# Optimization experiments

Measured on AMD Instinct MI355X. Metric: run time of the kernel, lower is better.

The kernel has to match this reference:

```python
import jax, jax.numpy as jnp
import numpy as np

ALIGN_CORNERS = True
APPLY_SMOOTHSTEP = True

SIZES = [(32, 32, 32), (64, 64, 64), (128, 128, 128), (256, 256, 256)]
FEAT_DIMS = [4, 4, 4, 4]
N_POINTS = 1048576  # 2**20 sample points (e.g. 8192 rays x 128 samples)


def setup_inputs() -> dict:
    key = jax.random.key(0)
    ks = jax.random.split(key, 1 + len(SIZES))
    # grid_sample-style coords in [-1, 1], layout [1, 1, 1, N, 3] (x, y, z)
    grid = jax.random.uniform(ks[0], (1, 1, 1, N_POINTS, 3), dtype=jnp.float32) * 2.0 - 1.0
    inp = {"grid": grid}
    for i, (size, c) in enumerate(zip(SIZES, FEAT_DIMS)):
        # original init: (rand(1,C,1,1,1)*2-1).repeat over spatial; use randn volumes for a
        # non-degenerate baseline (same shapes/math path)
        inp[f"vol{i}"] = jax.random.normal(ks[1 + i], (1, c, *size), dtype=jnp.float32)
    return inp


def _smooth_sample(vol, grid_pts):
    """Trilinear sample with border padding, align_corners=True, smoothstep weights.

    vol: [C, D, H, W]; grid_pts: [P, 3] with (x, y, z) in [-1, 1].
    Returns [C, P].
    """
    C, D, H, W = vol.shape
    # unnormalize (align_corners=True): [-1,1] -> [0, dim-1]; border padding via clip
    x = jnp.clip((grid_pts[:, 0] + 1.0) * 0.5 * (W - 1), 0.0, W - 1)
    y = jnp.clip((grid_pts[:, 1] + 1.0) * 0.5 * (H - 1), 0.0, H - 1)
    z = jnp.clip((grid_pts[:, 2] + 1.0) * 0.5 * (D - 1), 0.0, D - 1)

    x0 = jnp.floor(x); y0 = jnp.floor(y); z0 = jnp.floor(z)
    tx = x - x0; ty = y - y0; tz = z - z0
    if APPLY_SMOOTHSTEP:
        tx = tx * tx * (3.0 - 2.0 * tx)
        ty = ty * ty * (3.0 - 2.0 * ty)
        tz = tz * tz * (3.0 - 2.0 * tz)

    x0i = x0.astype(jnp.int32); x1i = jnp.minimum(x0i + 1, W - 1)
    y0i = y0.astype(jnp.int32); y1i = jnp.minimum(y0i + 1, H - 1)
    z0i = z0.astype(jnp.int32); z1i = jnp.minimum(z0i + 1, D - 1)

    # 8 corner gathers -> [C, P]
    c000 = vol[:, z0i, y0i, x0i]; c001 = vol[:, z0i, y0i, x1i]
    c010 = vol[:, z0i, y1i, x0i]; c011 = vol[:, z0i, y1i, x1i]
    c100 = vol[:, z1i, y0i, x0i]; c101 = vol[:, z1i, y0i, x1i]
    c110 = vol[:, z1i, y1i, x0i]; c111 = vol[:, z1i, y1i, x1i]

    c00 = c000 + (c001 - c000) * tx
    c01 = c010 + (c011 - c010) * tx
    c10 = c100 + (c101 - c100) * tx
    c11 = c110 + (c111 - c110) * tx
    c0 = c00 + (c01 - c00) * ty
    c1 = c10 + (c11 - c10) * ty
    return c0 + (c1 - c0) * tz


def reference(grid, vol0, vol1, vol2, vol3):
    # grid: [1, 1, 1, N, 3] -> [N, 3]
    pts = grid.reshape(-1, 3)
    n = pts.shape[0]
    out = []
    for vol in (vol0, vol1, vol2, vol3):
        feat = _smooth_sample(vol[0], pts)            # [C, N]
        out.append(feat.reshape(1, -1, 1, 1, n))      # grid_sample output layout
    return jnp.concatenate(out, axis=1)               # [1, sum(C), 1, 1, N]
```

## Files before the change

kernel.cpp:

```cpp
#include <hip/hip_runtime.h>

#define NPTS 1048576

#define DHW0 (32 * 32 * 32)
#define DHW1 (64 * 64 * 64)
#define DHW2 (128 * 128 * 128)
#define DHW3 (256 * 256 * 256)

typedef float v4f __attribute__((ext_vector_type(4)));

__device__ __forceinline__ void nt_store4(const float4 f, float4* p) {
    __builtin_nontemporal_store(*(const v4f*)&f, (v4f*)p);
}


__device__ __forceinline__ float4 lerp4(const float4 a, const float4 b, const float t) {
    return make_float4(a.x + (b.x - a.x) * t,
                       a.y + (b.y - a.y) * t,
                       a.z + (b.z - a.z) * t,
                       a.w + (b.w - a.w) * t);
}

struct CoordW { float tx, ty, tz; int b00, b01, b10, b11, x0, x1; };

template<int D>
__device__ __forceinline__ CoordW mkcoord(float gx, float gy, float gz) {
    CoordW c;
    float x = fminf(fmaxf((gx + 1.0f) * (0.5f * (float)(D - 1)), 0.0f), (float)(D - 1));
    float y = fminf(fmaxf((gy + 1.0f) * (0.5f * (float)(D - 1)), 0.0f), (float)(D - 1));
    float z = fminf(fmaxf((gz + 1.0f) * (0.5f * (float)(D - 1)), 0.0f), (float)(D - 1));
    float xf = floorf(x), yf = floorf(y), zf = floorf(z);
    float tx = x - xf, ty = y - yf, tz = z - zf;
    c.tx = tx * tx * (3.0f - 2.0f * tx);
    c.ty = ty * ty * (3.0f - 2.0f * ty);
    c.tz = tz * tz * (3.0f - 2.0f * tz);
    int x0 = (int)xf, y0 = (int)yf, z0 = (int)zf;
    int y1 = min(y0 + 1, D - 1), z1 = min(z0 + 1, D - 1);
    c.x0 = x0;
    c.x1 = min(x0 + 1, D - 1);
    c.b00 = (z0 * D + y0) * D;
    c.b01 = (z0 * D + y1) * D;
    c.b10 = (z1 * D + y0) * D;
    c.b11 = (z1 * D + y1) * D;
    return c;
}

__device__ __forceinline__ float4 reduce8(const float4* q, const CoordW& c) {
    float4 c00 = lerp4(q[0], q[1], c.tx);
    float4 c01 = lerp4(q[2], q[3], c.tx);
    float4 c10 = lerp4(q[4], q[5], c.tx);
    float4 c11 = lerp4(q[6], q[7], c.tx);
    float4 c0 = lerp4(c00, c01, c.ty);
    float4 c1 = lerp4(c10, c11, c.ty);
    return lerp4(c0, c1, c.tz);
}

__device__ __forceinline__ float4 reduce_v3(const float2* qd, const CoordW& c, bool edge) {
    float r[4];
#pragma unroll
    for (int ch = 0; ch < 4; ++ch) {
        float v00a = edge ? qd[ch * 4 + 0].y : qd[ch * 4 + 0].x, v00b = qd[ch * 4 + 0].y;
        float v01a = edge ? qd[ch * 4 + 1].y : qd[ch * 4 + 1].x, v01b = qd[ch * 4 + 1].y;
        float v10a = edge ? qd[ch * 4 + 2].y : qd[ch * 4 + 2].x, v10b = qd[ch * 4 + 2].y;
        float v11a = edge ? qd[ch * 4 + 3].y : qd[ch * 4 + 3].x, v11b = qd[ch * 4 + 3].y;
        float c00 = v00a + (v00b - v00a) * c.tx;
        float c01 = v01a + (v01b - v01a) * c.tx;
        float c10 = v10a + (v10b - v10a) * c.tx;
        float c11 = v11a + (v11b - v11a) * c.tx;
        float e0 = c00 + (c01 - c00) * c.ty;
        float e1 = c10 + (c11 - c10) * c.ty;
        r[ch] = e0 + (e1 - e0) * c.tz;
    }
    return make_float4(r[0], r[1], r[2], r[3]);
}

__device__ __forceinline__ void store16(const float4 f0, const float4 f1,
                                        const float4 f2, const float4 f3,
                                        float* __restrict__ out, int p) {
    __builtin_nontemporal_store(f0.x, &out[ 0 * NPTS + p]);
    __builtin_nontemporal_store(f0.y, &out[ 1 * NPTS + p]);
    __builtin_nontemporal_store(f0.z, &out[ 2 * NPTS + p]);
    __builtin_nontemporal_store(f0.w, &out[ 3 * NPTS + p]);
    __builtin_nontemporal_store(f1.x, &out[ 4 * NPTS + p]);
    __builtin_nontemporal_store(f1.y, &out[ 5 * NPTS + p]);
    __builtin_nontemporal_store(f1.z, &out[ 6 * NPTS + p]);
    __builtin_nontemporal_store(f1.w, &out[ 7 * NPTS + p]);
    __builtin_nontemporal_store(f2.x, &out[ 8 * NPTS + p]);
    __builtin_nontemporal_store(f2.y, &out[ 9 * NPTS + p]);
    __builtin_nontemporal_store(f2.z, &out[10 * NPTS + p]);
    __builtin_nontemporal_store(f2.w, &out[11 * NPTS + p]);
    __builtin_nontemporal_store(f3.x, &out[12 * NPTS + p]);
    __builtin_nontemporal_store(f3.y, &out[13 * NPTS + p]);
    __builtin_nontemporal_store(f3.z, &out[14 * NPTS + p]);
    __builtin_nontemporal_store(f3.w, &out[15 * NPTS + p]);
}


__global__ __launch_bounds__(256) void xpose_kernel(
    const float* __restrict__ v0, const float* __restrict__ v1,
    const float* __restrict__ v2, const float* __restrict__ v3,
    float4* __restrict__ w0, float4* __restrict__ w1,
    float4* __restrict__ w2, float4* __restrict__ w3)
{
    constexpr int B2 = DHW2 / 256, B1 = DHW1 / 256, B0 = DHW0 / 256;
    int b = blockIdx.x;
    int t = threadIdx.x;
    if (b < B2) {
        int v = b * 256 + t;
        w2[v] = make_float4(v2[v], v2[v + DHW2], v2[v + 2 * DHW2], v2[v + 3 * DHW2]);
    } else if (b < B2 + B1) {
        int v = (b - B2) * 256 + t;
        w1[v] = make_float4(v1[v], v1[v + DHW1], v1[v + 2 * DHW1], v1[v + 3 * DHW1]);
    } else if (b < B2 + B1 + B0) {
        int v = (b - B2 - B1) * 256 + t;
        w0[v] = make_float4(v0[v], v0[v + DHW0], v0[v + 2 * DHW0], v0[v + 3 * DHW0]);
    } else {
        int v = (b - B2 - B1 - B0) * 256 + t;
        nt_store4(make_float4(v3[v], v3[v + DHW3], v3[v + 2 * DHW3], v3[v + 3 * DHW3]),
                  w3 + v);
    }
}


__global__ __launch_bounds__(256, 3) void mg_fused_kernel(
    const float* __restrict__ grid,
    const float4* __restrict__ w0, const float4* __restrict__ w1,
    const float4* __restrict__ w2, const float* __restrict__ v3,
    float* __restrict__ out)
{
    int p = blockIdx.x * 256 + (int)threadIdx.x;
    float gx = grid[3 * p + 0];
    float gy = grid[3 * p + 1];
    float gz = grid[3 * p + 2];

    CoordW c0 = mkcoord<32>(gx, gy, gz);
    CoordW c1 = mkcoord<64>(gx, gy, gz);
    CoordW c2 = mkcoord<128>(gx, gy, gz);
    CoordW c3 = mkcoord<256>(gx, gy, gz);
    const int  xm = min(c3.x0, 254);
    const bool edge = (c3.x0 == 255);

    float4 qa[8], qb[8], qc[8];
    float2 qd[16];

    qa[0] = w0[c0.b00 + c0.x0]; qa[1] = w0[c0.b00 + c0.x1];
    qa[2] = w0[c0.b01 + c0.x0]; qa[3] = w0[c0.b01 + c0.x1];
    qa[4] = w0[c0.b10 + c0.x0]; qa[5] = w0[c0.b10 + c0.x1];
    qa[6] = w0[c0.b11 + c0.x0]; qa[7] = w0[c0.b11 + c0.x1];

    qb[0] = w1[c1.b00 + c1.x0]; qb[1] = w1[c1.b00 + c1.x1];
    qb[2] = w1[c1.b01 + c1.x0]; qb[3] = w1[c1.b01 + c1.x1];
    qb[4] = w1[c1.b10 + c1.x0]; qb[5] = w1[c1.b10 + c1.x1];
    qb[6] = w1[c1.b11 + c1.x0]; qb[7] = w1[c1.b11 + c1.x1];

    qc[0] = w2[c2.b00 + c2.x0]; qc[1] = w2[c2.b00 + c2.x1];
    qc[2] = w2[c2.b01 + c2.x0]; qc[3] = w2[c2.b01 + c2.x1];
    qc[4] = w2[c2.b10 + c2.x0]; qc[5] = w2[c2.b10 + c2.x1];
    qc[6] = w2[c2.b11 + c2.x0]; qc[7] = w2[c2.b11 + c2.x1];

#pragma unroll
    for (int ch = 0; ch < 4; ++ch) {
        const float* __restrict__ vc = v3 + (size_t)ch * DHW3;
        qd[ch * 4 + 0] = *(const float2*)(vc + c3.b00 + xm);
        qd[ch * 4 + 1] = *(const float2*)(vc + c3.b01 + xm);
        qd[ch * 4 + 2] = *(const float2*)(vc + c3.b10 + xm);
        qd[ch * 4 + 3] = *(const float2*)(vc + c3.b11 + xm);
    }

    __builtin_amdgcn_sched_barrier(0);

    float4 f0 = reduce8(qa, c0);
    float4 f1 = reduce8(qb, c1);
    float4 f2 = reduce8(qc, c2);
    float4 f3 = reduce_v3(qd, c3, edge);

    store16(f0, f1, f2, f3, out, p);
}


__global__ __launch_bounds__(256, 3) void mg_fused_w3_kernel(
    const float* __restrict__ grid,
    const float4* __restrict__ w0, const float4* __restrict__ w1,
    const float4* __restrict__ w2, const float4* __restrict__ w3,
    float* __restrict__ out)
{
    int p = blockIdx.x * 256 + (int)threadIdx.x;
    float gx = grid[3 * p + 0];
    float gy = grid[3 * p + 1];
    float gz = grid[3 * p + 2];

    CoordW c0 = mkcoord<32>(gx, gy, gz);
    CoordW c1 = mkcoord<64>(gx, gy, gz);
    CoordW c2 = mkcoord<128>(gx, gy, gz);
    CoordW c3 = mkcoord<256>(gx, gy, gz);
    const int  xm = min(c3.x0, 254);
    const bool edge = (c3.x0 == 255);

    float4 qa[8], qb[8], qc[8], qlo[4], qhi[4];

    qa[0] = w0[c0.b00 + c0.x0]; qa[1] = w0[c0.b00 + c0.x1];
    qa[2] = w0[c0.b01 + c0.x0]; qa[3] = w0[c0.b01 + c0.x1];
    qa[4] = w0[c0.b10 + c0.x0]; qa[5] = w0[c0.b10 + c0.x1];
    qa[6] = w0[c0.b11 + c0.x0]; qa[7] = w0[c0.b11 + c0.x1];

    qb[0] = w1[c1.b00 + c1.x0]; qb[1] = w1[c1.b00 + c1.x1];
    qb[2] = w1[c1.b01 + c1.x0]; qb[3] = w1[c1.b01 + c1.x1];
    qb[4] = w1[c1.b10 + c1.x0]; qb[5] = w1[c1.b10 + c1.x1];
    qb[6] = w1[c1.b11 + c1.x0]; qb[7] = w1[c1.b11 + c1.x1];

    qc[0] = w2[c2.b00 + c2.x0]; qc[1] = w2[c2.b00 + c2.x1];
    qc[2] = w2[c2.b01 + c2.x0]; qc[3] = w2[c2.b01 + c2.x1];
    qc[4] = w2[c2.b10 + c2.x0]; qc[5] = w2[c2.b10 + c2.x1];
    qc[6] = w2[c2.b11 + c2.x0]; qc[7] = w2[c2.b11 + c2.x1];

    qlo[0] = w3[c3.b00 + xm]; qhi[0] = w3[c3.b00 + xm + 1];
    qlo[1] = w3[c3.b01 + xm]; qhi[1] = w3[c3.b01 + xm + 1];
    qlo[2] = w3[c3.b10 + xm]; qhi[2] = w3[c3.b10 + xm + 1];
    qlo[3] = w3[c3.b11 + xm]; qhi[3] = w3[c3.b11 + xm + 1];

    __builtin_amdgcn_sched_barrier(0);

    float4 f0 = reduce8(qa, c0);
    float4 f1 = reduce8(qb, c1);
    float4 f2 = reduce8(qc, c2);

    float4 a00 = edge ? qhi[0] : qlo[0];
    float4 a01 = edge ? qhi[1] : qlo[1];
    float4 a10 = edge ? qhi[2] : qlo[2];
    float4 a11 = edge ? qhi[3] : qlo[3];
    float4 r00 = lerp4(a00, qhi[0], c3.tx);
    float4 r01 = lerp4(a01, qhi[1], c3.tx);
    float4 r10 = lerp4(a10, qhi[2], c3.tx);
    float4 r11 = lerp4(a11, qhi[3], c3.tx);
    float4 e0 = lerp4(r00, r01, c3.ty);
    float4 e1 = lerp4(r10, r11, c3.ty);
    float4 f3 = lerp4(e0, e1, c3.tz);

    store16(f0, f1, f2, f3, out, p);
}


template<int D>
__device__ __forceinline__ float4 sample_direct(const float* __restrict__ v,
                                                float gx, float gy, float gz) {
    CoordW c = mkcoord<D>(gx, gy, gz);
    float r[4];
#pragma unroll
    for (int ch = 0; ch < 4; ++ch) {
        const float* __restrict__ vc = v + (size_t)ch * (D * D * D);
        float c000 = vc[c.b00 + c.x0], c001 = vc[c.b00 + c.x1];
        float c010 = vc[c.b01 + c.x0], c011 = vc[c.b01 + c.x1];
        float c100 = vc[c.b10 + c.x0], c101 = vc[c.b10 + c.x1];
        float c110 = vc[c.b11 + c.x0], c111 = vc[c.b11 + c.x1];
        float c00 = c000 + (c001 - c000) * c.tx;
        float c01 = c010 + (c011 - c010) * c.tx;
        float c10 = c100 + (c101 - c100) * c.tx;
        float c11 = c110 + (c111 - c110) * c.tx;
        float e0 = c00 + (c01 - c00) * c.ty;
        float e1 = c10 + (c11 - c10) * c.ty;
        r[ch] = e0 + (e1 - e0) * c.tz;
    }
    return make_float4(r[0], r[1], r[2], r[3]);
}

__global__ __launch_bounds__(256) void mg_direct_kernel(
    const float* __restrict__ grid,
    const float* __restrict__ v0, const float* __restrict__ v1,
    const float* __restrict__ v2, const float* __restrict__ v3,
    float* __restrict__ out)
{
    int p = blockIdx.x * blockDim.x + threadIdx.x;
    float gx = grid[3 * p + 0];
    float gy = grid[3 * p + 1];
    float gz = grid[3 * p + 2];
    float4 f0 = sample_direct<32>(v0, gx, gy, gz);
    float4 f1 = sample_direct<64>(v1, gx, gy, gz);
    float4 f2 = sample_direct<128>(v2, gx, gy, gz);
    float4 f3 = sample_direct<256>(v3, gx, gy, gz);
    store16(f0, f1, f2, f3, out, p);
}


extern "C" void kernel_launch(void* const* d_in, const int* in_sizes, int n_in,
                              void* d_out, int out_size, void* d_ws, size_t ws_size,
                              hipStream_t stream) {
    const float* grid = (const float*)d_in[0];
    const float* v0   = (const float*)d_in[1];
    const float* v1   = (const float*)d_in[2];
    const float* v2   = (const float*)d_in[3];
    const float* v3   = (const float*)d_in[4];
    float* out = (float*)d_out;

    constexpr size_t WS_INTER = (size_t)(DHW0 + DHW1 + DHW2) * 16;
    constexpr size_t WS_W3    = WS_INTER + (size_t)DHW3 * 16;

    const int threads = 256;
    const int pt_blocks = NPTS / threads;
    constexpr int xb_small = (DHW0 + DHW1 + DHW2) / 256;
    constexpr int xb_v3    = DHW3 / 256;

    if (ws_size >= WS_W3) {
        float4* w0 = (float4*)d_ws;
        float4* w1 = w0 + DHW0;
        float4* w2 = w1 + DHW1;
        float4* w3 = w2 + DHW2;
        xpose_kernel<<<xb_small + xb_v3, threads, 0, stream>>>(
            v0, v1, v2, v3, w0, w1, w2, w3);
        mg_fused_w3_kernel<<<pt_blocks, threads, 0, stream>>>(
            grid, w0, w1, w2, w3, out);
    } else if (ws_size >= WS_INTER) {
        float4* w0 = (float4*)d_ws;
        float4* w1 = w0 + DHW0;
        float4* w2 = w1 + DHW1;
        xpose_kernel<<<xb_small, threads, 0, stream>>>(
            v0, v1, v2, v3, w0, w1, w2, (float4*)nullptr);
        mg_fused_kernel<<<pt_blocks, threads, 0, stream>>>(
            grid, w0, w1, w2, v3, out);
    } else {
        mg_direct_kernel<<<pt_blocks, threads, 0, stream>>>(grid, v0, v1, v2, v3, out);
    }
}
```

Measured before the change: 680.1 us.

## Split fused sampler into big-level and small-level kernels, drop v3 transpose

The fused four-level sampling kernel becomes two kernels: one samples levels 2 and 3 (the 128^3 and 256^3 volumes), the other samples levels 0 and 1. Each kernel needs fewer registers, so both now request 4 blocks per SM instead of 3. The transposed copy of the 256^3 volume is no longer built; level 3 is read directly as float2 pairs from the original per-channel layout, which removes a 1 GB-scale transpose pass. The cost is reading the grid coordinates twice and launching one extra kernel, and each level-3 sample now needs four separate channel-strided loads.

```diff
diff --git a/kernel.cpp b/kernel.cpp
--- a/kernel.cpp
+++ b/kernel.cpp
@@ -8,10 +8,6 @@
 #define DHW3 (256 * 256 * 256)
 
 typedef float v4f __attribute__((ext_vector_type(4)));
-
-__device__ __forceinline__ void nt_store4(const float4 f, float4* p) {
-    __builtin_nontemporal_store(*(const v4f*)&f, (v4f*)p);
-}
 
 
 __device__ __forceinline__ float4 lerp4(const float4 a, const float4 b, const float t) {
@@ -74,35 +70,32 @@
     return make_float4(r[0], r[1], r[2], r[3]);
 }
 
+__device__ __forceinline__ void store8(const float4 fa, const float4 fb,
+                                       float* __restrict__ out, int p) {
+    __builtin_nontemporal_store(fa.x, &out[0 * NPTS + p]);
+    __builtin_nontemporal_store(fa.y, &out[1 * NPTS + p]);
+    __builtin_nontemporal_store(fa.z, &out[2 * NPTS + p]);
+    __builtin_nontemporal_store(fa.w, &out[3 * NPTS + p]);
+    __builtin_nontemporal_store(fb.x, &out[4 * NPTS + p]);
+    __builtin_nontemporal_store(fb.y, &out[5 * NPTS + p]);
+    __builtin_nontemporal_store(fb.z, &out[6 * NPTS + p]);
+    __builtin_nontemporal_store(fb.w, &out[7 * NPTS + p]);
+}
+
 __device__ __forceinline__ void store16(const float4 f0, const float4 f1,
                                         const float4 f2, const float4 f3,
                                         float* __restrict__ out, int p) {
-    __builtin_nontemporal_store(f0.x, &out[ 0 * NPTS + p]);
-    __builtin_nontemporal_store(f0.y, &out[ 1 * NPTS + p]);
-    __builtin_nontemporal_store(f0.z, &out[ 2 * NPTS + p]);
-    __builtin_nontemporal_store(f0.w, &out[ 3 * NPTS + p]);
-    __builtin_nontemporal_store(f1.x, &out[ 4 * NPTS + p]);
-    __builtin_nontemporal_store(f1.y, &out[ 5 * NPTS + p]);
-    __builtin_nontemporal_store(f1.z, &out[ 6 * NPTS + p]);
-    __builtin_nontemporal_store(f1.w, &out[ 7 * NPTS + p]);
-    __builtin_nontemporal_store(f2.x, &out[ 8 * NPTS + p]);
-    __builtin_nontemporal_store(f2.y, &out[ 9 * NPTS + p]);
-    __builtin_nontemporal_store(f2.z, &out[10 * NPTS + p]);
-    __builtin_nontemporal_store(f2.w, &out[11 * NPTS + p]);
-    __builtin_nontemporal_store(f3.x, &out[12 * NPTS + p]);
-    __builtin_nontemporal_store(f3.y, &out[13 * NPTS + p]);
-    __builtin_nontemporal_store(f3.z, &out[14 * NPTS + p]);
-    __builtin_nontemporal_store(f3.w, &out[15 * NPTS + p]);
+    store8(f0, f1, out, p);
+    store8(f2, f3, out + 8 * NPTS, p);
 }
 
 
 __global__ __launch_bounds__(256) void xpose_kernel(
     const float* __restrict__ v0, const float* __restrict__ v1,
-    const float* __restrict__ v2, const float* __restrict__ v3,
-    float4* __restrict__ w0, float4* __restrict__ w1,
-    float4* __restrict__ w2, float4* __restrict__ w3)
-{
-    constexpr int B2 = DHW2 / 256, B1 = DHW1 / 256, B0 = DHW0 / 256;
+    const float* __restrict__ v2,
+    float4* __restrict__ w0, float4* __restrict__ w1, float4* __restrict__ w2)
+{
+    constexpr int B2 = DHW2 / 256, B1 = DHW1 / 256;
     int b = blockIdx.x;
     int t = threadIdx.x;
     if (b < B2) {
@@ -111,21 +104,16 @@
     } else if (b < B2 + B1) {
         int v = (b - B2) * 256 + t;
         w1[v] = make_float4(v1[v], v1[v + DHW1], v1[v + 2 * DHW1], v1[v + 3 * DHW1]);
-    } else if (b < B2 + B1 + B0) {
+    } else {
         int v = (b - B2 - B1) * 256 + t;
         w0[v] = make_float4(v0[v], v0[v + DHW0], v0[v + 2 * DHW0], v0[v + 3 * DHW0]);
-    } else {
-        int v = (b - B2 - B1 - B0) * 256 + t;
-        nt_store4(make_float4(v3[v], v3[v + DHW3], v3[v + 2 * DHW3], v3[v + 3 * DHW3]),
-                  w3 + v);
-    }
-}
-
-
-__global__ __launch_bounds__(256, 3) void mg_fused_kernel(
+    }
+}
+
+
+__global__ __launch_bounds__(256, 4) void mg_small_kernel(
     const float* __restrict__ grid,
     const float4* __restrict__ w0, const float4* __restrict__ w1,
-    const float4* __restrict__ w2, const float* __restrict__ v3,
     float* __restrict__ out)
 {
     int p = blockIdx.x * 256 + (int)threadIdx.x;
@@ -135,23 +123,42 @@
 
     CoordW c0 = mkcoord<32>(gx, gy, gz);
     CoordW c1 = mkcoord<64>(gx, gy, gz);
+
+    float4 qa[8], qb[8];
+    qa[0] = w0[c0.b00 + c0.x0]; qa[1] = w0[c0.b00 + c0.x1];
+    qa[2] = w0[c0.b01 + c0.x0]; qa[3] = w0[c0.b01 + c0.x1];
+    qa[4] = w0[c0.b10 + c0.x0]; qa[5] = w0[c0.b10 + c0.x1];
+    qa[6] = w0[c0.b11 + c0.x0]; qa[7] = w0[c0.b11 + c0.x1];
+
+    qb[0] = w1[c1.b00 + c1.x0]; qb[1] = w1[c1.b00 + c1.x1];
+    qb[2] = w1[c1.b01 + c1.x0]; qb[3] = w1[c1.b01 + c1.x1];
+    qb[4] = w1[c1.b10 + c1.x0]; qb[5] = w1[c1.b10 + c1.x1];
+    qb[6] = w1[c1.b11 + c1.x0]; qb[7] = w1[c1.b11 + c1.x1];
+
+    __builtin_amdgcn_sched_barrier(0);
+
+    float4 f0 = reduce8(qa, c0);
+    float4 f1 = reduce8(qb, c1);
+    store8(f0, f1, out, p);
+}
+
+__global__ __launch_bounds__(256, 4) void mg_big_kernel(
+    const float* __restrict__ grid,
+    const float4* __restrict__ w2, const float* __restrict__ v3,
+    float* __restrict__ out)
+{
+    int p = blockIdx.x * 256 + (int)threadIdx.x;
+    float gx = grid[3 * p + 0];
+    float gy = grid[3 * p + 1];
+    float gz = grid[3 * p + 2];
+
     CoordW c2 = mkcoord<128>(gx, gy, gz);
     CoordW c3 = mkcoord<256>(gx, gy, gz);
     const int  xm = min(c3.x0, 254);
     const bool edge = (c3.x0 == 255);
 
-    float4 qa[8], qb[8], qc[8];
+    float4 qc[8];
     float2 qd[16];
-
-    qa[0] = w0[c0.b00 + c0.x0]; qa[1] = w0[c0.b00 + c0.x1];
-    qa[2] = w0[c0.b01 + c0.x0]; qa[3] = w0[c0.b01 + c0.x1];
-    qa[4] = w0[c0.b10 + c0.x0]; qa[5] = w0[c0.b10 + c0.x1];
-    qa[6] = w0[c0.b11 + c0.x0]; qa[7] = w0[c0.b11 + c0.x1];
-
-    qb[0] = w1[c1.b00 + c1.x0]; qb[1] = w1[c1.b00 + c1.x1];
-    qb[2] = w1[c1.b01 + c1.x0]; qb[3] = w1[c1.b01 + c1.x1];
-    qb[4] = w1[c1.b10 + c1.x0]; qb[5] = w1[c1.b10 + c1.x1];
-    qb[6] = w1[c1.b11 + c1.x0]; qb[7] = w1[c1.b11 + c1.x1];
 
     qc[0] = w2[c2.b00 + c2.x0]; qc[1] = w2[c2.b00 + c2.x1];
     qc[2] = w2[c2.b01 + c2.x0]; qc[3] = w2[c2.b01 + c2.x1];
@@ -169,74 +176,9 @@
 
     __builtin_amdgcn_sched_barrier(0);
 
-    float4 f0 = reduce8(qa, c0);
-    float4 f1 = reduce8(qb, c1);
     float4 f2 = reduce8(qc, c2);
     float4 f3 = reduce_v3(qd, c3, edge);
-
-    store16(f0, f1, f2, f3, out, p);
-}
-
-
-__global__ __launch_bounds__(256, 3) void mg_fused_w3_kernel(
-    const float* __restrict__ grid,
-    const float4* __restrict__ w0, const float4* __restrict__ w1,
-    const float4* __restrict__ w2, const float4* __restrict__ w3,
-    float* __restrict__ out)
-{
-    int p = blockIdx.x * 256 + (int)threadIdx.x;
-    float gx = grid[3 * p + 0];
-    float gy = grid[3 * p + 1];
-    float gz = grid[3 * p + 2];
-
-    CoordW c0 = mkcoord<32>(gx, gy, gz);
-    CoordW c1 = mkcoord<64>(gx, gy, gz);
-    CoordW c2 = mkcoord<128>(gx, gy, gz);
-    CoordW c3 = mkcoord<256>(gx, gy, gz);
-    const int  xm = min(c3.x0, 254);
-    const bool edge = (c3.x0 == 255);
-
-    float4 qa[8], qb[8], qc[8], qlo[4], qhi[4];
-
-    qa[0] = w0[c0.b00 + c0.x0]; qa[1] = w0[c0.b00 + c0.x1];
-    qa[2] = w0[c0.b01 + c0.x0]; qa[3] = w0[c0.b01 + c0.x1];
-    qa[4] = w0[c0.b10 + c0.x0]; qa[5] = w0[c0.b10 + c0.x1];
-    qa[6] = w0[c0.b11 + c0.x0]; qa[7] = w0[c0.b11 + c0.x1];
-
-    qb[0] = w1[c1.b00 + c1.x0]; qb[1] = w1[c1.b00 + c1.x1];
-    qb[2] = w1[c1.b01 + c1.x0]; qb[3] = w1[c1.b01 + c1.x1];
-    qb[4] = w1[c1.b10 + c1.x0]; qb[5] = w1[c1.b10 + c1.x1];
-    qb[6] = w1[c1.b11 + c1.x0]; qb[7] = w1[c1.b11 + c1.x1];
-
-    qc[0] = w2[c2.b00 + c2.x0]; qc[1] = w2[c2.b00 + c2.x1];
-    qc[2] = w2[c2.b01 + c2.x0]; qc[3] = w2[c2.b01 + c2.x1];
-    qc[4] = w2[c2.b10 + c2.x0]; qc[5] = w2[c2.b10 + c2.x1];
-    qc[6] = w2[c2.b11 + c2.x0]; qc[7] = w2[c2.b11 + c2.x1];
-
-    qlo[0] = w3[c3.b00 + xm]; qhi[0] = w3[c3.b00 + xm + 1];
-    qlo[1] = w3[c3.b01 + xm]; qhi[1] = w3[c3.b01 + xm + 1];
-    qlo[2] = w3[c3.b10 + xm]; qhi[2] = w3[c3.b10 + xm + 1];
-    qlo[3] = w3[c3.b11 + xm]; qhi[3] = w3[c3.b11 + xm + 1];
-
-    __builtin_amdgcn_sched_barrier(0);
-
-    float4 f0 = reduce8(qa, c0);
-    float4 f1 = reduce8(qb, c1);
-    float4 f2 = reduce8(qc, c2);
-
-    float4 a00 = edge ? qhi[0] : qlo[0];
-    float4 a01 = edge ? qhi[1] : qlo[1];
-    float4 a10 = edge ? qhi[2] : qlo[2];
-    float4 a11 = edge ? qhi[3] : qlo[3];
-    float4 r00 = lerp4(a00, qhi[0], c3.tx);
-    float4 r01 = lerp4(a01, qhi[1], c3.tx);
-    float4 r10 = lerp4(a10, qhi[2], c3.tx);
-    float4 r11 = lerp4(a11, qhi[3], c3.tx);
-    float4 e0 = lerp4(r00, r01, c3.ty);
-    float4 e1 = lerp4(r10, r11, c3.ty);
-    float4 f3 = lerp4(e0, e1, c3.tz);
-
-    store16(f0, f1, f2, f3, out, p);
+    store8(f2, f3, out + 8 * NPTS, p);
 }
 
 
@@ -292,30 +234,18 @@
     float* out = (float*)d_out;
 
     constexpr size_t WS_INTER = (size_t)(DHW0 + DHW1 + DHW2) * 16;
-    constexpr size_t WS_W3    = WS_INTER + (size_t)DHW3 * 16;
 
     const int threads = 256;
     const int pt_blocks = NPTS / threads;
     constexpr int xb_small = (DHW0 + DHW1 + DHW2) / 256;
-    constexpr int xb_v3    = DHW3 / 256;
-
-    if (ws_size >= WS_W3) {
+
+    if (ws_size >= WS_INTER) {
         float4* w0 = (float4*)d_ws;
         float4* w1 = w0 + DHW0;
         float4* w2 = w1 + DHW1;
-        float4* w3 = w2 + DHW2;
-        xpose_kernel<<<xb_small + xb_v3, threads, 0, stream>>>(
-            v0, v1, v2, v3, w0, w1, w2, w3);
-        mg_fused_w3_kernel<<<pt_blocks, threads, 0, stream>>>(
-            grid, w0, w1, w2, w3, out);
-    } else if (ws_size >= WS_INTER) {
-        float4* w0 = (float4*)d_ws;
-        float4* w1 = w0 + DHW0;
-        float4* w2 = w1 + DHW1;
-        xpose_kernel<<<xb_small, threads, 0, stream>>>(
-            v0, v1, v2, v3, w0, w1, w2, (float4*)nullptr);
-        mg_fused_kernel<<<pt_blocks, threads, 0, stream>>>(
-            grid, w0, w1, w2, v3, out);
+        xpose_kernel<<<xb_small, threads, 0, stream>>>(v0, v1, v2, w0, w1, w2);
+        mg_big_kernel<<<pt_blocks, threads, 0, stream>>>(grid, w2, v3, out);
+        mg_small_kernel<<<pt_blocks, threads, 0, stream>>>(grid, w0, w1, out);
     } else {
         mg_direct_kernel<<<pt_blocks, threads, 0, stream>>>(grid, v0, v1, v2, v3, out);
     }
```

New measurement: 799.3 us. 1.18x slower.
